# Kernel tuning notes

Hardware: AMD Instinct MI355X
Metric: run time of the kernel (lower is better)

## Reference

```python
import jax, jax.numpy as jnp
import numpy as np

V, E, H, C = 50000, 300, 1024, 13
FEAT = E + 7 + 12  # layer0 input size = embedding_dim + casing(7) + pos(12)


def setup_inputs() -> dict:
    key = jax.random.key(0)
    ks = jax.random.split(key, 16)
    T, B = 256, 256
    std = 1.0 / np.sqrt(H)

    def unif(k, shape):
        return jax.random.uniform(k, shape, jnp.float32, -std, std)

    return {
        "tokens": jax.random.randint(ks[0], (T, B), 0, V, dtype=jnp.int32),
        "casing": jax.random.normal(ks[1], (T, B, 7), jnp.float32),
        "pos": jax.random.normal(ks[2], (T, B, 12), jnp.float32),
        "emb_table": jax.random.normal(ks[3], (V, E), jnp.float32) * 0.1,  # frozen embeddings
        "wi0": unif(ks[4], (4 * H, FEAT)), "bi0": unif(ks[5], (4 * H,)),
        "wh0": unif(ks[6], (4 * H, H)),   "bh0": unif(ks[7], (4 * H,)),
        "wi1": unif(ks[8], (4 * H, H)),   "bi1": unif(ks[9], (4 * H,)),
        "wh1": unif(ks[10], (4 * H, H)),  "bh1": unif(ks[11], (4 * H,)),
        "dec_w": unif(ks[12], (C, 2 * H)), "dec_b": unif(ks[13], (C,)),
        "h_init": jnp.zeros((2, B, H), jnp.float32),
        "c_init": jnp.zeros((2, B, H), jnp.float32),
    }


def _lstm_cell(x, h, c, wi, bi, wh, bh):
    # preact = i2h(x) + h2h(h); gate order per source: i, f, o, g (g is 4th chunk)
    pre = x @ wi.T + bi + h @ wh.T + bh  # [B, 4H]
    i = jax.nn.sigmoid(pre[:, :H])
    f = jax.nn.sigmoid(pre[:, H:2 * H])
    o = jax.nn.sigmoid(pre[:, 2 * H:3 * H])
    g = jnp.tanh(pre[:, 3 * H:])
    c_t = f * c + i * g
    h_t = o * jnp.tanh(c_t)
    return h_t, c_t


def reference(tokens, casing, pos, emb_table, wi0, bi0, wh0, bh0,
              wi1, bi1, wh1, bh1, dec_w, dec_b, h_init, c_init):
    # Eval path: embedding / variational / weight dropout are identity.
    x_emb = emb_table[tokens]                                # [T,B,E]
    x = jnp.concatenate([x_emb, casing, pos], axis=-1)       # [T,B,FEAT]

    def step(carry, xt):
        h0, c0, _, _ = carry
        h0n, c0n = _lstm_cell(xt, h0, c0, wi0, bi0, wh0, bh0)
        # layer1's recurrent state is the batch-flipped layer0 state (per source)
        h1n, c1n = _lstm_cell(h0n, h0n[::-1], c0n[::-1], wi1, bi1, wh1, bh1)
        return (h0n, c0n, h1n, c1n), jnp.concatenate([h0n, h1n], axis=1)

    carry0 = (h_init[0], c_init[0], h_init[1], c_init[1])
    _, outs = jax.lax.scan(step, carry0, x)                  # [T,B,2H]
    T, B = outs.shape[0], outs.shape[1]
    decoded = outs.reshape(T * B, 2 * H) @ dec_w.T + dec_b   # [T*B, C]
    return decoded
```

## Files before the change

### kernel.cpp

```cpp
#include <hip/hip_runtime.h>
#include <stdint.h>


typedef __attribute__((ext_vector_type(8))) short bf16x8;
typedef __attribute__((ext_vector_type(4))) float f32x4;

#define SLOT 262144ull

__device__ __forceinline__ uint16_t f2bf(float f) {
  uint32_t u = __float_as_uint(f);
  u += 0x7fffu + ((u >> 16) & 1u);
  return (uint16_t)(u >> 16);
}
__device__ __forceinline__ float bf2f(uint16_t h) {
  return __uint_as_float(((uint32_t)h) << 16);
}
__device__ __forceinline__ float sigmoidf_(float x) {
  return __builtin_amdgcn_rcpf(1.0f + __expf(-x));
}
__device__ __forceinline__ float tanhf_(float x) {
  return 1.0f - 2.0f * __builtin_amdgcn_rcpf(__expf(2.0f * x) + 1.0f);
}
__device__ __forceinline__ void gload_lds16(const void* g, void* l) {
  __builtin_amdgcn_global_load_lds(
      (const __attribute__((address_space(1))) void*)g,
      (__attribute__((address_space(3))) void*)l, 16, 0, 0);
}
__device__ __forceinline__ bf16x8 lds_frag(const uint16_t* base, int row, int kc) {
  const uint16_t* p = base + row * 32 + ((kc ^ ((row >> 1) & 3)) << 3);
  return *(const bf16x8*)p;
}
__device__ __forceinline__ f32x4 mfma16(bf16x8 a, bf16x8 b, f32x4 c) {
  return __builtin_amdgcn_mfma_f32_16x16x32_bf16(a, b, c, 0, 0, 0);
}

__global__ __launch_bounds__(256) void k_prep_w0(
    const float* __restrict__ wi0, const float* __restrict__ bi0,
    const float* __restrict__ wh0, const float* __restrict__ bh0,
    uint16_t* __restrict__ W0c, float* __restrict__ b0) {
  int r = blockIdx.x;
  int p = r & 3, j = r >> 2;
  int src = p * 1024 + j;
  const float* wi = wi0 + (size_t)src * 319;
  const float* wh = wh0 + (size_t)src * 1024;
  uint16_t* dst = W0c + (size_t)r * 1344;
  for (int k = threadIdx.x; k < 1344; k += 256) {
    float v;
    if (k < 319) v = wi[k];
    else if (k == 319) v = 0.0f;
    else v = wh[k - 320];
    dst[k] = f2bf(v);
  }
  if (threadIdx.x == 0) b0[r] = bi0[src] + bh0[src];
}

__global__ __launch_bounds__(256) void k_prep_w1(
    const float* __restrict__ wi1, const float* __restrict__ bi1,
    const float* __restrict__ wh1, const float* __restrict__ bh1,
    uint16_t* __restrict__ W1c, float* __restrict__ b1) {
  int r = blockIdx.x;
  int p = r & 3, j = r >> 2;
  int src = p * 1024 + j;
  const float* wi = wi1 + (size_t)src * 1024;
  const float* wh = wh1 + (size_t)src * 1024;
  uint16_t* dst = W1c + (size_t)r * 2048;
  for (int k = threadIdx.x; k < 2048; k += 256) {
    float v = (k < 1024) ? wi[k] : wh[k - 1024];
    dst[k] = f2bf(v);
  }
  if (threadIdx.x == 0) b1[r] = bi1[src] + bh1[src];
}

__global__ __launch_bounds__(256) void k_init(
    const float* __restrict__ h_init, const float* __restrict__ c_init,
    uint16_t* __restrict__ h_slot, float* __restrict__ c_state) {
  int i = blockIdx.x * 256 + threadIdx.x;
  h_slot[i] = f2bf(h_init[i]);
  c_state[i] = c_init[i];
}

__global__ __launch_bounds__(256) void k_embed(
    const int* __restrict__ tokens, const float* __restrict__ casing,
    const float* __restrict__ pos, const float* __restrict__ emb,
    uint16_t* __restrict__ x_bf) {
  int row = blockIdx.x * 4 + (threadIdx.x >> 6);
  int l = threadIdx.x & 63;
  int tok = tokens[row];
  const float* er = emb + (size_t)tok * 300;
  uint16_t* xr = x_bf + (size_t)row * 320;
#pragma unroll
  for (int c0 = 0; c0 < 320; c0 += 64) {
    int c = c0 + l;
    float v;
    if (c < 300) v = er[c];
    else if (c < 307) v = casing[(size_t)row * 7 + (c - 300)];
    else if (c < 319) v = pos[(size_t)row * 12 + (c - 307)];
    else v = 0.0f;
    xr[c] = f2bf(v);
  }
}

__global__ __launch_bounds__(256, 4) void k_step(
    const uint16_t* __restrict__ x_t, const uint16_t* __restrict__ W0c,
    const float* __restrict__ b0, const uint16_t* __restrict__ h_in,
    uint16_t* __restrict__ h_out, uint16_t* __restrict__ c0_out,
    float* __restrict__ c_state) {
  __shared__ __align__(16) uint16_t As[4][1024];
  __shared__ __align__(16) uint16_t Bs[4][1024];
  __shared__ __align__(16) float epi[4][16][20];
  int tid = threadIdx.x;
  int w = tid >> 6, l = tid & 63;
  int wr = w >> 1, wc = w & 1;
  int lid = (blockIdx.x & 7) * 128 + (blockIdx.x >> 3);
  int Mb = (lid & 7) * 32;
  int Nb = (lid >> 3) * 32;
  f32x4 acc = {};

  int sc = (l & 3) ^ ((l >> 3) & 3);
  const uint16_t* xrow =
      x_t + (size_t)(Mb + (w & 1) * 16 + (l >> 2)) * 320 + sc * 8;
  const uint16_t* hrow =
      h_in + (size_t)(Mb + (w & 1) * 16 + (l >> 2)) * 1024 + sc * 8;
  const uint16_t* wrow =
      W0c + (size_t)(Nb + (w & 1) * 16 + (l >> 2)) * 1344 + sc * 8;

  auto stage = [&](int kt, int buf) {
    int kg = kt * 32;
    if (w < 2) {
      const uint16_t* sA = (kt < 10) ? (xrow + kg) : (hrow + (kg - 320));
      gload_lds16(sA, &As[buf][w * 512]);
    } else {
      gload_lds16(wrow + kg, &Bs[buf][(w & 1) * 512]);
    }
  };

  stage(0, 0);
  stage(1, 1);
  stage(2, 2);
  for (int kt = 0; kt < 42; ++kt) {
    __builtin_amdgcn_sched_barrier(0);
    if (kt < 40) asm volatile("s_waitcnt vmcnt(2)" ::: "memory");
    else if (kt == 40) asm volatile("s_waitcnt vmcnt(1)" ::: "memory");
    else asm volatile("s_waitcnt vmcnt(0)" ::: "memory");
    __builtin_amdgcn_s_barrier();
    __builtin_amdgcn_sched_barrier(0);
    if (kt < 39) stage(kt + 3, (kt + 3) & 3);
    const uint16_t* Ab = As[kt & 3];
    const uint16_t* Bb = Bs[kt & 3];
    bf16x8 a0 = lds_frag(Ab, wr * 16 + (l & 15), l >> 4);
    bf16x8 q0 = lds_frag(Bb, wc * 16 + (l & 15), l >> 4);
    acc = mfma16(a0, q0, acc);
  }

  int jbase = (Nb + wc * 16) >> 2;
#pragma unroll
  for (int r = 0; r < 4; ++r)
    epi[w][(l >> 4) * 4 + r][l & 15] = acc[r];
  asm volatile("s_waitcnt lgkmcnt(0)" ::: "memory");
  {
    int rr = l >> 2, j = l & 3;
    f32x4 q = *(const f32x4*)&epi[w][rr][j * 4];
    f32x4 bv = *(const f32x4*)&b0[(jbase + j) * 4];
    float vi = sigmoidf_(q[0] + bv[0]);
    float vf = sigmoidf_(q[1] + bv[1]);
    float vo = sigmoidf_(q[2] + bv[2]);
    float vg = tanhf_(q[3] + bv[3]);
    int bg = Mb + wr * 16 + rr;
    int jg = jbase + j;
    size_t sidx = (size_t)bg * 1024 + jg;
    float cold = c_state[sidx];
    float cn = vf * cold + vi * vg;
    float hh = vo * tanhf_(cn);
    c_state[sidx] = cn;
    c0_out[sidx] = f2bf(cn);
    h_out[sidx] = f2bf(hh);
  }
}

__global__ __launch_bounds__(256, 3) void k_l1gemm(
    const uint16_t* __restrict__ h0buf, const uint16_t* __restrict__ W1c,
    const float* __restrict__ b1, const uint16_t* __restrict__ c0buf,
    uint16_t* __restrict__ h1buf) {
  __shared__ __align__(16) char smem[49152];
  float* epif = (float*)smem;
  int tid = threadIdx.x;
  int w = tid >> 6, l = tid & 63;
  int wr = w >> 1, wc = w & 1;
  uint32_t G = gridDim.x;
  uint32_t cpx = G >> 3;
  uint32_t lid = (blockIdx.x & 7) * cpx + (blockIdx.x >> 3);
  uint32_t yyTot = G >> 5;
  uint32_t nb = lid / yyTot;
  uint32_t yy = lid - nb * yyTot;
  int Nb = (int)nb * 128;
  int tl = (int)(yy >> 1);
  int bbase = (int)(yy & 1) * 128;
  const uint16_t* hrow = h0buf + (size_t)tl * SLOT;
  const uint16_t* c0s = c0buf + (size_t)tl * SLOT;
  uint16_t* h1s = h1buf + (size_t)tl * SLOT;
  f32x4 acc[4][4] = {};

  int sc = (l & 3) ^ ((l >> 3) & 3);
  int srow0 = (w * 2 + 0) * 16 + (l >> 2);
  int srow1 = (w * 2 + 1) * 16 + (l >> 2);
  const uint16_t* hA0n = hrow + (size_t)(bbase + srow0) * 1024;
  const uint16_t* hA0f = hrow + (size_t)(255 - (bbase + srow0)) * 1024;
  const uint16_t* hA1n = hrow + (size_t)(bbase + srow1) * 1024;
  const uint16_t* hA1f = hrow + (size_t)(255 - (bbase + srow1)) * 1024;
  const uint16_t* wB0 = W1c + (size_t)(Nb + srow0) * 2048;
  const uint16_t* wB1 = W1c + (size_t)(Nb + srow1) * 2048;

  auto stage = [&](int kt, int buf) {
    int kg = kt * 32 + sc * 8;
    const uint16_t* sA0 = (kg < 1024) ? (hA0n + kg) : (hA0f + (kg - 1024));
    const uint16_t* sA1 = (kg < 1024) ? (hA1n + kg) : (hA1f + (kg - 1024));
    char* base = smem + buf * 16384;
    gload_lds16(sA0, base + (w * 2 + 0) * 1024);
    gload_lds16(sA1, base + (w * 2 + 1) * 1024);
    gload_lds16(wB0 + kg, base + 8192 + (w * 2 + 0) * 1024);
    gload_lds16(wB1 + kg, base + 8192 + (w * 2 + 1) * 1024);
  };

  stage(0, 0);
  stage(1, 1);
  for (int kt = 0; kt < 64; ++kt) {
    __builtin_amdgcn_sched_barrier(0);
    if (kt < 63) asm volatile("s_waitcnt vmcnt(4)" ::: "memory");
    else asm volatile("s_waitcnt vmcnt(0)" ::: "memory");
    __builtin_amdgcn_s_barrier();
    __builtin_amdgcn_sched_barrier(0);
    if (kt < 62) stage(kt + 2, (kt + 2) % 3);
    const uint16_t* As = (const uint16_t*)(smem + (kt % 3) * 16384);
    const uint16_t* Bs = As + 4096;
    bf16x8 a[4], q[4];
#pragma unroll
    for (int m = 0; m < 4; ++m) a[m] = lds_frag(As, wr * 64 + m * 16 + (l & 15), l >> 4);
#pragma unroll
    for (int n = 0; n < 4; ++n) q[n] = lds_frag(Bs, wc * 64 + n * 16 + (l & 15), l >> 4);
#pragma unroll
    for (int m = 0; m < 4; ++m)
#pragma unroll
      for (int n = 0; n < 4; ++n) acc[m][n] = mfma16(a[m], q[n], acc[m][n]);
  }
  __syncthreads();

  int jbase = (Nb + wc * 64) >> 2;
#pragma unroll
  for (int m = 0; m < 4; ++m) {
#pragma unroll
    for (int n = 0; n < 4; ++n)
#pragma unroll
      for (int r = 0; r < 4; ++r)
        epif[((size_t)w * 16 + (l >> 4) * 4 + r) * 68 + n * 16 + (l & 15)] =
            acc[m][n][r];
    asm volatile("s_waitcnt lgkmcnt(0)" ::: "memory");
#pragma unroll
    for (int it = 0; it < 4; ++it) {
      int pp = it * 64 + l;
      int rr = pp >> 4, j = pp & 15;
      f32x4 q = *(const f32x4*)&epif[((size_t)w * 16 + rr) * 68 + j * 4];
      f32x4 bv = *(const f32x4*)&b1[(size_t)(jbase + j) * 4];
      float vi = sigmoidf_(q[0] + bv[0]);
      float vf = sigmoidf_(q[1] + bv[1]);
      float vo = sigmoidf_(q[2] + bv[2]);
      float vg = tanhf_(q[3] + bv[3]);
      int rowl = wr * 64 + m * 16 + rr;
      int b = bbase + rowl;
      int jg = jbase + j;
      float c0v = bf2f(c0s[(size_t)(255 - b) * 1024 + jg]);
      float cn = vf * c0v + vi * vg;
      float hh = vo * tanhf_(cn);
      h1s[(size_t)b * 1024 + jg] = f2bf(hh);
    }
    asm volatile("s_waitcnt lgkmcnt(0)" ::: "memory");
  }
}

__global__ __launch_bounds__(256) void k_decode(
    const uint16_t* __restrict__ h0buf, const uint16_t* __restrict__ h1buf,
    const float* __restrict__ dec_w, const float* __restrict__ dec_b,
    float* __restrict__ out, int t0) {
  int rowl = blockIdx.x * 4 + (threadIdx.x >> 6);
  int l = threadIdx.x & 63;
  int tl = rowl >> 8, b = rowl & 255;
  const uint16_t* h0 = h0buf + (size_t)tl * SLOT + (size_t)b * 1024;
  const uint16_t* h1 = h1buf + (size_t)tl * SLOT + (size_t)b * 1024;
  float acc[13];
#pragma unroll
  for (int c = 0; c < 13; ++c) acc[c] = 0.0f;
#pragma unroll
  for (int part = 0; part < 2; ++part) {
    const uint16_t* h = part ? h1 : h0;
    const float* wb = dec_w + part * 1024 + (size_t)l * 16;
    float hv[16];
    const bf16x8* hp = (const bf16x8*)(h + l * 16);
    bf16x8 v0 = hp[0];
    bf16x8 v1 = hp[1];
#pragma unroll
    for (int jj = 0; jj < 8; ++jj) {
      hv[jj] = bf2f((uint16_t)v0[jj]);
      hv[8 + jj] = bf2f((uint16_t)v1[jj]);
    }
#pragma unroll
    for (int c = 0; c < 13; ++c) {
      const float* wc = wb + (size_t)c * 2048;
      float s = 0.0f;
#pragma unroll
      for (int jj = 0; jj < 16; ++jj) s += hv[jj] * wc[jj];
      acc[c] += s;
    }
  }
#pragma unroll
  for (int c = 0; c < 13; ++c) {
    float v = acc[c];
#pragma unroll
    for (int off = 32; off > 0; off >>= 1) v += __shfl_xor(v, off, 64);
    acc[c] = v;
  }
  if (l == 0) {
    int t = t0 + tl;
    float* orow = out + ((size_t)t * 256 + b) * 13;
#pragma unroll
    for (int c = 0; c < 13; ++c) orow[c] = acc[c] + dec_b[c];
  }
}

extern "C" void kernel_launch(void* const* d_in, const int* in_sizes, int n_in,
                              void* d_out, int out_size, void* d_ws, size_t ws_size,
                              hipStream_t stream) {
  const int* tokens = (const int*)d_in[0];
  const float* casing = (const float*)d_in[1];
  const float* pos = (const float*)d_in[2];
  const float* emb = (const float*)d_in[3];
  const float* wi0 = (const float*)d_in[4];
  const float* bi0 = (const float*)d_in[5];
  const float* wh0 = (const float*)d_in[6];
  const float* bh0 = (const float*)d_in[7];
  const float* wi1 = (const float*)d_in[8];
  const float* bi1 = (const float*)d_in[9];
  const float* wh1 = (const float*)d_in[10];
  const float* bh1 = (const float*)d_in[11];
  const float* dec_w = (const float*)d_in[12];
  const float* dec_b = (const float*)d_in[13];
  const float* h_init = (const float*)d_in[14];
  const float* c_init = (const float*)d_in[15];
  float* out = (float*)d_out;
  (void)in_sizes; (void)n_in; (void)out_size;

  char* ws = (char*)d_ws;
  size_t off = 0;
  auto alloc = [&](size_t bytes) {
    char* p = ws + off;
    off += (bytes + 255) & ~(size_t)255;
    return p;
  };
  uint16_t* W0c = (uint16_t*)alloc(4096ull * 1344 * 2);
  float* b0 = (float*)alloc(4096 * 4);
  uint16_t* W1c = (uint16_t*)alloc(4096ull * 2048 * 2);
  float* b1 = (float*)alloc(4096 * 4);
  uint16_t* x_bf = (uint16_t*)alloc(65536ull * 320 * 2);
  float* c_st = (float*)alloc(SLOT * 4);

  const size_t SB = SLOT * 2;
  int CH = 0;
  for (int c = 64; c >= 2; c >>= 1) {
    if (off + (size_t)(3 * c + 1) * SB + 4096 <= ws_size) { CH = c; break; }
  }
  if (CH == 0) return;
  uint16_t* h0buf = (uint16_t*)alloc((size_t)(CH + 1) * SB);
  uint16_t* c0buf = (uint16_t*)alloc((size_t)CH * SB);
  uint16_t* h1buf = (uint16_t*)alloc((size_t)CH * SB);

  k_prep_w0<<<4096, 256, 0, stream>>>(wi0, bi0, wh0, bh0, W0c, b0);
  k_prep_w1<<<4096, 256, 0, stream>>>(wi1, bi1, wh1, bh1, W1c, b1);
  k_embed<<<16384, 256, 0, stream>>>(tokens, casing, pos, emb, x_bf);
  k_init<<<1024, 256, 0, stream>>>(h_init, c_init, h0buf + (size_t)CH * SLOT,
                                   c_st);

  for (int t0 = 0; t0 < 256; t0 += CH) {
    for (int tl = 0; tl < CH; ++tl) {
      int t = t0 + tl;
      int in_s = (tl > 0) ? (tl - 1) : ((t0 == 0) ? CH : CH - 1);
      k_step<<<1024, 256, 0, stream>>>(
          x_bf + (size_t)t * 81920, W0c, b0,
          h0buf + (size_t)in_s * SLOT,
          h0buf + (size_t)tl * SLOT,
          c0buf + (size_t)tl * SLOT, c_st);
    }
    k_l1gemm<<<64 * CH, 256, 0, stream>>>(h0buf, W1c, b1, c0buf, h1buf);
    k_decode<<<CH * 64, 256, 0, stream>>>(h0buf, h1buf, dec_w, dec_b, out, t0);
  }
}
```

Before: 4.696 ms.

## Split K of layer-0 step GEMM across two wave groups per block

```diff
diff --git a/kernel.cpp b/kernel.cpp
--- a/kernel.cpp
+++ b/kernel.cpp
@@ -100,17 +100,16 @@
   }
 }
 
-__global__ __launch_bounds__(256, 4) void k_step(
+__global__ __launch_bounds__(512, 8) void k_step(
     const uint16_t* __restrict__ x_t, const uint16_t* __restrict__ W0c,
     const float* __restrict__ b0, const uint16_t* __restrict__ h_in,
     uint16_t* __restrict__ h_out, uint16_t* __restrict__ c0_out,
     float* __restrict__ c_state) {
-  __shared__ __align__(16) uint16_t As[4][1024];
-  __shared__ __align__(16) uint16_t Bs[4][1024];
-  __shared__ __align__(16) float epi[4][16][20];
+  __shared__ __align__(16) char smem[32768];
   int tid = threadIdx.x;
   int w = tid >> 6, l = tid & 63;
-  int wr = w >> 1, wc = w & 1;
+  int kc = w >> 2, q = w & 3;
+  int wr = q >> 1, wc = q & 1;
   int lid = (blockIdx.x & 7) * 128 + (blockIdx.x >> 3);
   int Mb = (lid & 7) * 32;
   int Nb = (lid >> 3) * 32;
@@ -118,53 +117,60 @@
 
   int sc = (l & 3) ^ ((l >> 3) & 3);
   const uint16_t* xrow =
-      x_t + (size_t)(Mb + (w & 1) * 16 + (l >> 2)) * 320 + sc * 8;
+      x_t + (size_t)(Mb + (q & 1) * 16 + (l >> 2)) * 320 + sc * 8;
   const uint16_t* hrow =
-      h_in + (size_t)(Mb + (w & 1) * 16 + (l >> 2)) * 1024 + sc * 8;
+      h_in + (size_t)(Mb + (q & 1) * 16 + (l >> 2)) * 1024 + sc * 8;
   const uint16_t* wrow =
-      W0c + (size_t)(Nb + (w & 1) * 16 + (l >> 2)) * 1344 + sc * 8;
-
-  auto stage = [&](int kt, int buf) {
+      W0c + (size_t)(Nb + (q & 1) * 16 + (l >> 2)) * 1344 + sc * 8;
+  char* halfbase = smem + kc * 16384;
+
+  auto stage = [&](int i) {
+    int buf = i & 3;
+    int kt = kc * 21 + i;
     int kg = kt * 32;
-    if (w < 2) {
+    if (q < 2) {
       const uint16_t* sA = (kt < 10) ? (xrow + kg) : (hrow + (kg - 320));
-      gload_lds16(sA, &As[buf][w * 512]);
+      gload_lds16(sA, halfbase + buf * 2048 + q * 1024);
     } else {
-      gload_lds16(wrow + kg, &Bs[buf][(w & 1) * 512]);
+      gload_lds16(wrow + kg, halfbase + 8192 + buf * 2048 + (q - 2) * 1024);
     }
   };
 
-  stage(0, 0);
-  stage(1, 1);
-  stage(2, 2);
-  for (int kt = 0; kt < 42; ++kt) {
+  stage(0);
+  stage(1);
+  stage(2);
+  for (int i = 0; i < 21; ++i) {
     __builtin_amdgcn_sched_barrier(0);
-    if (kt < 40) asm volatile("s_waitcnt vmcnt(2)" ::: "memory");
-    else if (kt == 40) asm volatile("s_waitcnt vmcnt(1)" ::: "memory");
+    if (i < 19) asm volatile("s_waitcnt vmcnt(2)" ::: "memory");
+    else if (i == 19) asm volatile("s_waitcnt vmcnt(1)" ::: "memory");
     else asm volatile("s_waitcnt vmcnt(0)" ::: "memory");
     __builtin_amdgcn_s_barrier();
     __builtin_amdgcn_sched_barrier(0);
-    if (kt < 39) stage(kt + 3, (kt + 3) & 3);
-    const uint16_t* Ab = As[kt & 3];
-    const uint16_t* Bb = Bs[kt & 3];
+    if (i < 18) stage(i + 3);
+    const uint16_t* Ab = (const uint16_t*)(halfbase + (i & 3) * 2048);
+    const uint16_t* Bb = (const uint16_t*)(halfbase + 8192 + (i & 3) * 2048);
     bf16x8 a0 = lds_frag(Ab, wr * 16 + (l & 15), l >> 4);
     bf16x8 q0 = lds_frag(Bb, wc * 16 + (l & 15), l >> 4);
     acc = mfma16(a0, q0, acc);
   }
 
-  int jbase = (Nb + wc * 16) >> 2;
+  __syncthreads();
+  float* epif = (float*)smem;
 #pragma unroll
   for (int r = 0; r < 4; ++r)
-    epi[w][(l >> 4) * 4 + r][l & 15] = acc[r];
-  asm volatile("s_waitcnt lgkmcnt(0)" ::: "memory");
-  {
+    epif[((q * 2 + kc) * 16 + (l >> 4) * 4 + r) * 20 + (l & 15)] = acc[r];
+  __syncthreads();
+
+  if (kc == 0) {
     int rr = l >> 2, j = l & 3;
-    f32x4 q = *(const f32x4*)&epi[w][rr][j * 4];
+    int jbase = (Nb + wc * 16) >> 2;
+    f32x4 q0 = *(const f32x4*)&epif[((q * 2 + 0) * 16 + rr) * 20 + j * 4];
+    f32x4 q1 = *(const f32x4*)&epif[((q * 2 + 1) * 16 + rr) * 20 + j * 4];
     f32x4 bv = *(const f32x4*)&b0[(jbase + j) * 4];
-    float vi = sigmoidf_(q[0] + bv[0]);
-    float vf = sigmoidf_(q[1] + bv[1]);
-    float vo = sigmoidf_(q[2] + bv[2]);
-    float vg = tanhf_(q[3] + bv[3]);
+    float vi = sigmoidf_(q0[0] + q1[0] + bv[0]);
+    float vf = sigmoidf_(q0[1] + q1[1] + bv[1]);
+    float vo = sigmoidf_(q0[2] + q1[2] + bv[2]);
+    float vg = tanhf_(q0[3] + q1[3] + bv[3]);
     int bg = Mb + wr * 16 + rr;
     int jg = jbase + j;
     size_t sidx = (size_t)bg * 1024 + jg;
@@ -381,7 +387,7 @@
     for (int tl = 0; tl < CH; ++tl) {
       int t = t0 + tl;
       int in_s = (tl > 0) ? (tl - 1) : ((t0 == 0) ? CH : CH - 1);
-      k_step<<<1024, 256, 0, stream>>>(
+      k_step<<<1024, 512, 0, stream>>>(
           x_bf + (size_t)t * 81920, W0c, b0,
           h0buf + (size_t)in_s * SLOT,
           h0buf + (size_t)tl * SLOT,
```

Result: slower. 4.870 ms (+3.7%).
